# Kernel optimization log

Measured on AMD Instinct MI355X. Metric: run time of the kernel, lower is better.

The kernel has to match this reference:

```python
import jax, jax.numpy as jnp
import numpy as np

GAMMA = 2.0
MARGIN = 0.3
SCALE = 30.0
B, C = 4096, 32768


def setup_inputs() -> dict:
    key = jax.random.key(0)
    k1, k2 = jax.random.split(key)
    inputs = jax.random.normal(k1, (B, C), dtype=jnp.float32)
    targets = jax.random.randint(k2, (B,), 0, C, dtype=jnp.int64)
    return {"inputs": inputs, "targets": targets}


def reference(inputs, targets):
    # Row-wise L2 normalize (F.normalize with eps=1e-12)
    norm = jnp.maximum(jnp.linalg.norm(inputs, axis=1, keepdims=True), 1e-12)
    normalized = inputs / norm  # (B, C)

    rows = jnp.arange(inputs.shape[0])
    # cos(theta) at target class
    cos_theta = normalized[rows, targets]
    theta = jnp.arccos(jnp.clip(cos_theta, -1.0 + 1e-7, 1.0 - 1e-7))
    cos_theta_m = jnp.cos(theta + MARGIN)

    # scatter margin-adjusted cosine back, then scale
    logits = normalized.at[rows, targets].set(cos_theta_m) * SCALE  # (B, C)

    # cross-entropy (no smoothing, no class weights)
    logp = jax.nn.log_softmax(logits, axis=1)
    ce = -logp[rows, targets]  # (B,)

    pt = jnp.exp(-ce)
    loss = (1.0 - pt) ** GAMMA * ce
    return jnp.mean(loss)
```

## Files before the change

### kernel.cpp

```cpp
#include <hip/hip_runtime.h>
#include <math.h>

#define B_ROWS 4096
#define C_COLS 32768
#define BLOCK  512
#define NWAVES (BLOCK / 64)
#define NF4    (C_COLS / 4 / BLOCK)

typedef float v4f __attribute__((ext_vector_type(4)));

static_assert(NF4 * BLOCK * 4 == C_COLS, "tiling must cover the row exactly");

__device__ __forceinline__ float wave_reduce_sum(float v) {
    #pragma unroll
    for (int off = 32; off > 0; off >>= 1)
        v += __shfl_down(v, off, 64);
    return v;
}

__device__ __forceinline__ float block_reduce_sum(float v, float* red, int tid) {
    const int wid  = tid >> 6;
    const int lane = tid & 63;
    v = wave_reduce_sum(v);
    if (lane == 0) red[wid] = v;
    __syncthreads();
    if (wid == 0) {
        float s = (lane < NWAVES) ? red[lane] : 0.0f;
        #pragma unroll
        for (int off = NWAVES / 2; off > 0; off >>= 1)
            s += __shfl_down(s, off, 64);
        if (lane == 0) red[0] = s;
    }
    __syncthreads();
    return red[0];
}

__global__ __launch_bounds__(BLOCK, 4)
void focal_row_kernel(const float* __restrict__ inp,
                      const int*   __restrict__ tgt,
                      float*       __restrict__ row_loss) {
    constexpr float SCALE = 30.0f;
    constexpr float COSM  = 0.9553364891f;
    constexpr float SINM  = 0.2955202067f;

    const int row = blockIdx.x;
    const int tid = threadIdx.x;

    const v4f* __restrict__ rowp = (const v4f*)(inp + (size_t)row * C_COLS);

    __shared__ float red_a[NWAVES];
    __shared__ float red_b[NWAVES];

    float xt = 0.0f;
    if (tid == 0) {
        const int ct = tgt[row];
        xt = inp[(size_t)row * C_COLS + ct];
    }

    v4f r[NF4];
    #pragma unroll
    for (int k = 0; k < NF4; ++k)
        r[k] = __builtin_nontemporal_load(rowp + (k * BLOCK + tid));

    float s0 = 0.0f, s1 = 0.0f, s2 = 0.0f, s3 = 0.0f;
    #pragma unroll
    for (int k = 0; k < NF4; ++k) {
        s0 = fmaf(r[k].x, r[k].x, s0);
        s1 = fmaf(r[k].y, r[k].y, s1);
        s2 = fmaf(r[k].z, r[k].z, s2);
        s3 = fmaf(r[k].w, r[k].w, s3);
    }
    const float sumsq = (s0 + s1) + (s2 + s3);

    const float total_sq = block_reduce_sum(sumsq, red_a, tid);
    const float norm = fmaxf(sqrtf(total_sq), 1e-12f);
    const float inv  = SCALE / norm;

    float e0 = 0.0f, e1 = 0.0f, e2 = 0.0f, e3 = 0.0f;
    #pragma unroll
    for (int k = 0; k < NF4; ++k) {
        e0 += __expf(r[k].x * inv);
        e1 += __expf(r[k].y * inv);
        e2 += __expf(r[k].z * inv);
        e3 += __expf(r[k].w * inv);
    }
    const float se = (e0 + e1) + (e2 + e3);
    const float sumexp_full = block_reduce_sum(se, red_b, tid);

    if (tid == 0) {
        const float c  = xt / norm;
        const float cc = fminf(fmaxf(c, -1.0f + 1e-7f), 1.0f - 1e-7f);
        const float sin_t = sqrtf(fmaxf(1.0f - cc * cc, 0.0f));
        const float cosm  = cc * COSM - sin_t * SINM;
        const float lt    = SCALE * cosm;

        const float Z  = sumexp_full - __expf(SCALE * c) + __expf(lt);
        const float ce = logf(Z) - lt;
        const float pt = __expf(-ce);
        const float om = 1.0f - pt;
        row_loss[row] = om * om * ce;
    }
}

__global__ __launch_bounds__(1024)
void finalize_kernel(const float* __restrict__ row_loss,
                     float*       __restrict__ out) {
    const int tid = threadIdx.x;
    __shared__ float red[16];
    const int wid  = tid >> 6;
    const int lane = tid & 63;
    float s = 0.0f;
    #pragma unroll
    for (int k = 0; k < B_ROWS / 1024; ++k)
        s += row_loss[k * 1024 + tid];
    s = wave_reduce_sum(s);
    if (lane == 0) red[wid] = s;
    __syncthreads();
    if (wid == 0) {
        float t = (lane < 16) ? red[lane] : 0.0f;
        #pragma unroll
        for (int off = 8; off > 0; off >>= 1)
            t += __shfl_down(t, off, 64);
        if (lane == 0) out[0] = t * (1.0f / (float)B_ROWS);
    }
}

extern "C" void kernel_launch(void* const* d_in, const int* in_sizes, int n_in,
                              void* d_out, int out_size, void* d_ws, size_t ws_size,
                              hipStream_t stream) {
    const float* inp = (const float*)d_in[0];
    const int*   tgt = (const int*)d_in[1];
    float*       out = (float*)d_out;
    float*       row_loss = (float*)d_ws;

    focal_row_kernel<<<B_ROWS, BLOCK, 0, stream>>>(inp, tgt, row_loss);
    finalize_kernel<<<1, 1024, 0, stream>>>(row_loss, out);
}
```

Baseline: 636.8 us.

## Stream row twice instead of holding it in registers, raise occupancy

Stops caching the whole 128 KB row in registers (16 float4 per thread). The row is now read twice in loops of four float4 loads: once for the sum of squares and once for the exp sum. Launch bounds go from 4 to 8 blocks per CU. The aim is lower register pressure and more waves to hide memory latency. The cost is a second global read of each row, which relies on L2/MALL hits, and the nontemporal load hint is gone.

```diff
diff --git a/kernel.cpp b/kernel.cpp
--- a/kernel.cpp
+++ b/kernel.cpp
@@ -35,7 +35,7 @@
     return red[0];
 }
 
-__global__ __launch_bounds__(BLOCK, 4)
+__global__ __launch_bounds__(BLOCK, 8)
 void focal_row_kernel(const float* __restrict__ inp,
                       const int*   __restrict__ tgt,
                       float*       __restrict__ row_loss) {
@@ -57,18 +57,21 @@
         xt = inp[(size_t)row * C_COLS + ct];
     }
 
-    v4f r[NF4];
-    #pragma unroll
-    for (int k = 0; k < NF4; ++k)
-        r[k] = __builtin_nontemporal_load(rowp + (k * BLOCK + tid));
-
     float s0 = 0.0f, s1 = 0.0f, s2 = 0.0f, s3 = 0.0f;
-    #pragma unroll
-    for (int k = 0; k < NF4; ++k) {
-        s0 = fmaf(r[k].x, r[k].x, s0);
-        s1 = fmaf(r[k].y, r[k].y, s1);
-        s2 = fmaf(r[k].z, r[k].z, s2);
-        s3 = fmaf(r[k].w, r[k].w, s3);
+    #pragma unroll 1
+    for (int k = 0; k < NF4; k += 4) {
+        const v4f a0 = rowp[(k + 0) * BLOCK + tid];
+        const v4f a1 = rowp[(k + 1) * BLOCK + tid];
+        const v4f a2 = rowp[(k + 2) * BLOCK + tid];
+        const v4f a3 = rowp[(k + 3) * BLOCK + tid];
+        s0 = fmaf(a0.x, a0.x, s0); s1 = fmaf(a0.y, a0.y, s1);
+        s2 = fmaf(a0.z, a0.z, s2); s3 = fmaf(a0.w, a0.w, s3);
+        s0 = fmaf(a1.x, a1.x, s0); s1 = fmaf(a1.y, a1.y, s1);
+        s2 = fmaf(a1.z, a1.z, s2); s3 = fmaf(a1.w, a1.w, s3);
+        s0 = fmaf(a2.x, a2.x, s0); s1 = fmaf(a2.y, a2.y, s1);
+        s2 = fmaf(a2.z, a2.z, s2); s3 = fmaf(a2.w, a2.w, s3);
+        s0 = fmaf(a3.x, a3.x, s0); s1 = fmaf(a3.y, a3.y, s1);
+        s2 = fmaf(a3.z, a3.z, s2); s3 = fmaf(a3.w, a3.w, s3);
     }
     const float sumsq = (s0 + s1) + (s2 + s3);
 
@@ -77,12 +80,20 @@
     const float inv  = SCALE / norm;
 
     float e0 = 0.0f, e1 = 0.0f, e2 = 0.0f, e3 = 0.0f;
-    #pragma unroll
-    for (int k = 0; k < NF4; ++k) {
-        e0 += __expf(r[k].x * inv);
-        e1 += __expf(r[k].y * inv);
-        e2 += __expf(r[k].z * inv);
-        e3 += __expf(r[k].w * inv);
+    #pragma unroll 1
+    for (int k = 0; k < NF4; k += 4) {
+        const v4f a0 = rowp[(k + 0) * BLOCK + tid];
+        const v4f a1 = rowp[(k + 1) * BLOCK + tid];
+        const v4f a2 = rowp[(k + 2) * BLOCK + tid];
+        const v4f a3 = rowp[(k + 3) * BLOCK + tid];
+        e0 += __expf(a0.x * inv); e1 += __expf(a0.y * inv);
+        e2 += __expf(a0.z * inv); e3 += __expf(a0.w * inv);
+        e0 += __expf(a1.x * inv); e1 += __expf(a1.y * inv);
+        e2 += __expf(a1.z * inv); e3 += __expf(a1.w * inv);
+        e0 += __expf(a2.x * inv); e1 += __expf(a2.y * inv);
+        e2 += __expf(a2.z * inv); e3 += __expf(a2.w * inv);
+        e0 += __expf(a3.x * inv); e1 += __expf(a3.y * inv);
+        e2 += __expf(a3.z * inv); e3 += __expf(a3.w * inv);
     }
     const float se = (e0 + e1) + (e2 + e3);
     const float sumexp_full = block_reduce_sum(se, red_b, tid);
```

New measurement: 706.8 us. 1.11x slower.
